# Kernel tuning notes

Measured on AMD Instinct MI355X. Metric: run time of the kernel, lower is better.

Reference implementation:

```python
import jax, jax.numpy as jnp
import numpy as np
from jax import lax

N, H, W, C = 4, 64, 64, 256
G, K = 8, 3
Cg = C // G
PAD, STRIDE, DIL = 1, 1, 1
OFFSET_SCALE = 1.0
P = K * K


def setup_inputs() -> dict:
    key = jax.random.key(0)
    ks = jax.random.split(key, 12)
    s = 1.0 / np.sqrt(C)
    return {
        "x": jax.random.normal(ks[0], (N, H, W, C), jnp.float32),
        "in_w": jax.random.normal(ks[1], (C, C), jnp.float32) * s,
        "in_b": jnp.zeros((C,), jnp.float32),
        "out_w": jax.random.normal(ks[2], (C, C), jnp.float32) * s,
        "out_b": jnp.zeros((C,), jnp.float32),
        "off_w": jax.random.normal(ks[3], (C, G * P * 2), jnp.float32) * 0.02,
        "off_b": jax.random.normal(ks[4], (G * P * 2,), jnp.float32) * 0.1,
        "mask_w": jax.random.normal(ks[5], (C, G * P), jnp.float32) * 0.02,
        "mask_b": jnp.zeros((G * P,), jnp.float32),
        "dw_k": jax.random.normal(ks[6], (C, 1, K, K), jnp.float32) * (1.0 / K),
        "bn_g": 1.0 + 0.1 * jax.random.normal(ks[7], (C,), jnp.float32),
        "bn_b": 0.1 * jax.random.normal(ks[8], (C,), jnp.float32),
        "bn_m": 0.1 * jax.random.normal(ks[9], (C,), jnp.float32),
        "bn_v": 1.0 + 0.1 * jax.random.uniform(ks[10], (C,), jnp.float32),
    }


def _bilinear_sample(img, grid):
    # img: [B, Cc, Hi, Wi]; grid: [B, L, P, 2], (x, y) in [-1, 1]
    # grid_sample(mode='bilinear', padding_mode='zeros', align_corners=False)
    B, Cc, Hi, Wi = img.shape
    x = ((grid[..., 0] + 1.0) * Wi - 1.0) * 0.5
    y = ((grid[..., 1] + 1.0) * Hi - 1.0) * 0.5
    x0 = jnp.floor(x)
    y0 = jnp.floor(y)
    fx = x - x0
    fy = y - y0
    x0i = x0.astype(jnp.int32)
    y0i = y0.astype(jnp.int32)
    flat = img.reshape(B, Cc, Hi * Wi)
    gather = jax.vmap(lambda f, i: f[:, i])  # [Cc,HW], [L,P] -> [Cc,L,P]

    def corner(xc, yc, w):
        valid = (xc >= 0) & (xc < Wi) & (yc >= 0) & (yc < Hi)
        idx = jnp.clip(yc, 0, Hi - 1) * Wi + jnp.clip(xc, 0, Wi - 1)
        return gather(flat, idx) * (w * valid)[:, None]

    out = corner(x0i, y0i, (1.0 - fx) * (1.0 - fy))
    out = out + corner(x0i + 1, y0i, fx * (1.0 - fy))
    out = out + corner(x0i, y0i + 1, (1.0 - fx) * fy)
    out = out + corner(x0i + 1, y0i + 1, fx * fy)
    return out  # [B, Cc, L, P]


def reference(x, in_w, in_b, out_w, out_b, off_w, off_b, mask_w, mask_b,
              dw_k, bn_g, bn_b, bn_m, bn_v):
    # input_proj
    xp = x @ in_w + in_b  # [N,H,W,C]

    # depthwise conv (Conv: conv -> BN(inference) -> SiLU) on NCHW
    x1 = jnp.transpose(x, (0, 3, 1, 2))
    x1 = lax.conv_general_dilated(x1, dw_k, (1, 1), [(PAD, PAD), (PAD, PAD)],
                                  feature_group_count=C)
    x1 = (bn_g[:, None, None] * (x1 - bn_m[:, None, None])
          * lax.rsqrt(bn_v + 1e-5)[:, None, None] + bn_b[:, None, None])
    x1 = jax.nn.silu(x1)
    x1 = jnp.transpose(x1, (0, 2, 3, 1))  # NHWC

    offset = x1 @ off_w + off_b  # [N,H,W,G*P*2]
    mask = jax.nn.softmax((x1 @ mask_w + mask_b).reshape(N, H, W, G, P), -1)

    # dcnv3 core: pad input, compute sampling locations, bilinear gather
    Hi, Wi = H + 2 * PAD, W + 2 * PAD
    xpad = jnp.pad(xp, ((0, 0), (PAD, PAD), (PAD, PAD), (0, 0)))

    base = (DIL * (K - 1)) // 2 + 0.5
    ref_y = (base + jnp.arange(H, dtype=jnp.float32) * STRIDE) / Hi
    ref_x = (base + jnp.arange(W, dtype=jnp.float32) * STRIDE) / Wi
    ref = jnp.stack(jnp.meshgrid(ref_x, ref_y, indexing="xy"), -1)  # [H,W,2]

    g1 = jnp.arange(K, dtype=jnp.float32) * DIL - (DIL * (K - 1)) // 2
    gx = jnp.repeat(g1 / Wi, K)  # kx outer (torch meshgrid 'ij' order)
    gy = jnp.tile(g1 / Hi, K)    # ky inner
    grid = jnp.stack([gx, gy], -1)  # [P,2]

    norm = jnp.array([Wi, Hi], jnp.float32)
    loc = (ref[None, :, :, None, None, :]
           + grid[None, None, None, None, :, :] * OFFSET_SCALE
           + offset.reshape(N, H, W, G, P, 2) * (OFFSET_SCALE / norm))
    sgrid = 2.0 * loc - 1.0  # [N,H,W,G,P,2]

    img = xpad.reshape(N, Hi * Wi, G, Cg).transpose(0, 2, 3, 1).reshape(N * G, Cg, Hi, Wi)
    sg = sgrid.reshape(N, H * W, G, P, 2).transpose(0, 2, 1, 3, 4).reshape(N * G, H * W, P, 2)
    samples = _bilinear_sample(img, sg)  # [N*G, Cg, L, P]
    m = mask.reshape(N, H * W, G, P).transpose(0, 2, 1, 3).reshape(N * G, 1, H * W, P)
    out = (samples * m).sum(-1)  # [N*G, Cg, L]
    out = out.reshape(N, C, H * W).transpose(0, 2, 1).reshape(N, H, W, C)
    return out @ out_w + out_b
```

## Files before the change

kernel.cpp:

```cpp
#include <hip/hip_runtime.h>
#include <math.h>

#define NB   4
#define HH   64
#define WW   64
#define CCH  256
#define GG   8
#define CGC  32
#define HI   66
#define NPIX 16384
#define OMWS 256

typedef unsigned short ushort_t;
typedef __attribute__((ext_vector_type(8))) short short8;
typedef __attribute__((ext_vector_type(4))) float floatx4;

__device__ inline ushort_t f2bf(float f) {
    union { float f; unsigned u; } v; v.f = f;
    unsigned r = v.u + 0x7FFF + ((v.u >> 16) & 1);
    return (ushort_t)(r >> 16);
}
__device__ inline float bf2f(ushort_t u) {
    union { unsigned u; float f; } v; v.u = ((unsigned)u) << 16; return v.f;
}

__device__ inline void gload_lds16(const ushort_t* g, ushort_t* l) {
    __builtin_amdgcn_global_load_lds(
        (const __attribute__((address_space(1))) void*)g,
        (__attribute__((address_space(3))) void*)l, 16, 0, 0);
}

template<int MODE>
__device__ __forceinline__
void gemm_body(const ushort_t* __restrict__ A, const ushort_t* __restrict__ Bt,
               const float* __restrict__ bias, void* __restrict__ outv,
               ushort_t* As, ushort_t* Bs, int row0, int col0)
{
    const int tid  = threadIdx.x;
    const int lane = tid & 63, wid = tid >> 6;
    const int q = lane >> 4, r = lane & 15;

    floatx4 acc[2][4] = {};

    auto stage = [&](int buf, int kt) {
        #pragma unroll
        for (int j = 0; j < 4; ++j) {
            int gi = j * 256 + tid;
            int arow = gi >> 3, gk = gi & 7;
            gload_lds16(A + (size_t)(row0 + arow) * 256 + kt * 64 + ((gk ^ (arow & 7)) * 8),
                        &As[buf * 128 * 64 + gi * 8]);
        }
        #pragma unroll
        for (int j = 0; j < 2; ++j) {
            int gi = j * 256 + tid;
            int brow = gi >> 3, gk = gi & 7;
            gload_lds16(Bt + (size_t)(col0 + brow) * 256 + kt * 64 + ((gk ^ (brow & 7)) * 8),
                        &Bs[buf * 64 * 64 + gi * 8]);
        }
    };

    stage(0, 0);
    __syncthreads();
    int cur = 0;
    #pragma unroll 1
    for (int kt = 0; kt < 4; ++kt) {
        if (kt < 3) stage(cur ^ 1, kt + 1);
        #pragma unroll
        for (int kk = 0; kk < 2; ++kk) {
            short8 af[2], bf[4];
            const int gsw = ((kk * 4 + q) ^ (r & 7)) * 8;
            #pragma unroll
            for (int m = 0; m < 2; ++m)
                af[m] = *(const short8*)&As[cur * 128 * 64 + (wid * 32 + m * 16 + r) * 64 + gsw];
            #pragma unroll
            for (int n = 0; n < 4; ++n)
                bf[n] = *(const short8*)&Bs[cur * 64 * 64 + (n * 16 + r) * 64 + gsw];
            #pragma unroll
            for (int m = 0; m < 2; ++m)
                #pragma unroll
                for (int n = 0; n < 4; ++n)
                    acc[m][n] = __builtin_amdgcn_mfma_f32_16x16x32_bf16(
                                    af[m], bf[n], acc[m][n], 0, 0, 0);
        }
        __syncthreads();
        cur ^= 1;
    }

    #pragma unroll
    for (int m = 0; m < 2; ++m) {
        #pragma unroll
        for (int n = 0; n < 4; ++n) {
            #pragma unroll
            for (int j = 0; j < 4; ++j) {
                int row = row0 + wid * 32 + m * 16 + q * 4 + j;
                int col = col0 + n * 16 + r;
                float v = acc[m][n][j] + bias[col];
                if (MODE == 1) {
                    int nn = row >> 12, hh = (row >> 6) & 63, www = row & 63;
                    ((ushort_t*)outv)[(size_t)((nn * HI + hh + 1) * HI + (www + 1)) * CCH + col] = f2bf(v);
                } else if (MODE == 2) {
                    ((ushort_t*)outv)[(size_t)row * 256 + col] = f2bf(v);
                } else {
                    ((float*)outv)[(size_t)row * 256 + col] = v;
                }
            }
        }
    }
}

__device__ __forceinline__ void swz512(int tbid, int& row0, int& col0) {
    int swz = (tbid & 7) * 64 + (tbid >> 3);
    row0 = (swz >> 2) * 128;
    col0 = (swz & 3) * 64;
}

__global__ __launch_bounds__(256)
void gemm_in_off(const ushort_t* __restrict__ xb, const ushort_t* __restrict__ WtIn,
                 const float* __restrict__ in_b, ushort_t* __restrict__ xpadb,
                 const ushort_t* __restrict__ x1b, const ushort_t* __restrict__ W2t,
                 const float* __restrict__ b2, ushort_t* __restrict__ offm)
{
    __shared__ ushort_t As[2 * 128 * 64];
    __shared__ ushort_t Bs[2 * 64 * 64];
    int bid = blockIdx.x;
    int row0, col0;
    if (bid < 512) {
        swz512(bid, row0, col0);
        gemm_body<1>(xb, WtIn, in_b, xpadb, As, Bs, row0, col0);
    } else {
        swz512(bid - 512, row0, col0);
        gemm_body<2>(x1b, W2t, b2, offm, As, Bs, row0, col0);
    }
}

__global__ __launch_bounds__(256)
void gemm_out(const ushort_t* __restrict__ A, const ushort_t* __restrict__ Bt,
              const float* __restrict__ bias, float* __restrict__ out)
{
    __shared__ ushort_t As[2 * 128 * 64];
    __shared__ ushort_t Bs[2 * 64 * 64];
    int row0, col0;
    swz512(blockIdx.x, row0, col0);
    gemm_body<0>(A, Bt, bias, out, As, Bs, row0, col0);
}

__global__ __launch_bounds__(256)
void prep_dw(const float* __restrict__ x,
             const float* __restrict__ in_w, const float* __restrict__ out_w,
             const float* __restrict__ off_w, const float* __restrict__ mask_w,
             const float* __restrict__ off_b, const float* __restrict__ mask_b,
             const float* __restrict__ dw_k, const float* __restrict__ bn_g,
             const float* __restrict__ bn_b, const float* __restrict__ bn_m,
             const float* __restrict__ bn_v,
             ushort_t* __restrict__ xpadb,
             ushort_t* __restrict__ WtIn, ushort_t* __restrict__ WtOut,
             ushort_t* __restrict__ W2t, float* __restrict__ b2,
             ushort_t* __restrict__ x1b, ushort_t* __restrict__ xb)
{
    __shared__ float kT[9][256];
    const int bid = blockIdx.x;
    const int tid = threadIdx.x;

    if (bid < NB * 260) {
        int n = bid / 260, rp = bid % 260;
        int h, w;
        if (rp < 66)       { h = 0;              w = rp; }
        else if (rp < 132) { h = 65;             w = rp - 66; }
        else if (rp < 196) { h = 1 + (rp - 132); w = 0; }
        else               { h = 1 + (rp - 196); w = 65; }
        xpadb[(size_t)((n * HI + h) * HI + w) * CCH + tid] = 0;
        return;
    }
    if (bid < NB * 260 + 256) {
        int n = bid - NB * 260, k = tid;
        WtIn [n * 256 + k] = f2bf(in_w [k * 256 + n]);
        WtOut[n * 256 + k] = f2bf(out_w[k * 256 + n]);
        float w2 = (n < 144) ? off_w[k * 144 + n]
                 : (n < 216) ? mask_w[k * 72 + (n - 144)] : 0.f;
        W2t[n * 256 + k] = f2bf(w2);
        if (k == 0) b2[n] = (n < 144) ? off_b[n] : (n < 216) ? mask_b[n - 144] : 0.f;
        return;
    }

    #pragma unroll
    for (int j = 0; j < 9; ++j) {
        int i = j * 256 + tid;
        kT[i % 9][i / 9] = dw_k[i];
    }
    __syncthreads();

    const int lane = tid & 63, wvid = tid >> 6;
    const int pix = (bid - (NB * 260 + 256)) * 4 + wvid;
    const int n = pix >> 12, hw = pix & 4095, h = hw >> 6, w = hw & 63;
    const int c4 = lane << 2;

    const float4 cv = *reinterpret_cast<const float4*>(x + (size_t)pix * CCH + c4);
    ushort_t xo[4] = { f2bf(cv.x), f2bf(cv.y), f2bf(cv.z), f2bf(cv.w) };
    *reinterpret_cast<ushort4*>(xb + (size_t)pix * CCH + c4) = *reinterpret_cast<ushort4*>(xo);

    const float4 kc = *reinterpret_cast<const float4*>(&kT[4][c4]);
    float ax = cv.x * kc.x, ay = cv.y * kc.y, az = cv.z * kc.z, aw = cv.w * kc.w;

    #pragma unroll
    for (int tap = 0; tap < 9; ++tap) {
        if (tap == 4) continue;
        int hh = h + tap / 3 - 1, ww = w + tap % 3 - 1;
        if ((unsigned)hh < HH && (unsigned)ww < WW) {
            const float4 v = *reinterpret_cast<const float4*>(
                x + (size_t)((n * HH + hh) * WW + ww) * CCH + c4);
            const float4 kk = *reinterpret_cast<const float4*>(&kT[tap][c4]);
            ax += v.x * kk.x; ay += v.y * kk.y; az += v.z * kk.z; aw += v.w * kk.w;
        }
    }
    const float4 g4 = *reinterpret_cast<const float4*>(bn_g + c4);
    const float4 v4 = *reinterpret_cast<const float4*>(bn_v + c4);
    const float4 m4 = *reinterpret_cast<const float4*>(bn_m + c4);
    const float4 bb4 = *reinterpret_cast<const float4*>(bn_b + c4);
    float sx = g4.x * rsqrtf(v4.x + 1e-5f), sy = g4.y * rsqrtf(v4.y + 1e-5f);
    float sz = g4.z * rsqrtf(v4.z + 1e-5f), sw = g4.w * rsqrtf(v4.w + 1e-5f);
    float yx = (ax - m4.x) * sx + bb4.x, yy = (ay - m4.y) * sy + bb4.y;
    float yz = (az - m4.z) * sz + bb4.z, yw = (aw - m4.w) * sw + bb4.w;
    yx = yx / (1.f + __expf(-yx));
    yy = yy / (1.f + __expf(-yy));
    yz = yz / (1.f + __expf(-yz));
    yw = yw / (1.f + __expf(-yw));
    ushort_t o[4] = { f2bf(yx), f2bf(yy), f2bf(yz), f2bf(yw) };
    *reinterpret_cast<ushort4*>(x1b + (size_t)pix * CCH + c4) = *reinterpret_cast<ushort4*>(o);
}

__global__ __launch_bounds__(256)
void dcn_sample(const ushort_t* __restrict__ xpadb, const ushort_t* __restrict__ om,
                ushort_t* __restrict__ coreb)
{
    const int tid = threadIdx.x;
    const int pix = blockIdx.x * 8 + (tid >> 5);
    const int l   = tid & 31;
    const int g = l >> 2, c8 = (l & 3) << 3;
    const int n = pix >> 12, hw = pix & 4095, h = hw >> 6, w = hw & 63;
    const ushort_t* __restrict__ omp = om + (size_t)pix * OMWS;

    float lg[9], mx = -1e30f;
    #pragma unroll
    for (int p = 0; p < 9; ++p) { lg[p] = bf2f(omp[144 + g * 9 + p]); mx = fmaxf(mx, lg[p]); }
    float s = 0.f;
    #pragma unroll
    for (int p = 0; p < 9; ++p) { lg[p] = __expf(lg[p] - mx); s += lg[p]; }
    const float inv = 1.f / s;

    const ushort_t* __restrict__ img = xpadb + (size_t)n * HI * HI * CCH + g * CGC + c8;
    float acc[8] = {};
    #pragma unroll
    for (int p = 0; p < 9; ++p) {
        float ox = bf2f(omp[g * 18 + p * 2 + 0]);
        float oy = bf2f(omp[g * 18 + p * 2 + 1]);
        float xi = (float)(w + (p / 3)) + ox;
        float yi = (float)(h + (p % 3)) + oy;
        float x0f = floorf(xi), y0f = floorf(yi);
        int x0 = (int)x0f, y0 = (int)y0f;
        float fx = xi - x0f, fy = yi - y0f;
        float wgt = lg[p] * inv;
        float cw[4] = { (1.f - fx) * (1.f - fy) * wgt, fx * (1.f - fy) * wgt,
                        (1.f - fx) * fy * wgt,         fx * fy * wgt };
        #pragma unroll
        for (int cr = 0; cr < 4; ++cr) {
            int xc = x0 + (cr & 1), yc = y0 + (cr >> 1);
            if ((unsigned)xc < HI && (unsigned)yc < HI) {
                short8 raw = *reinterpret_cast<const short8*>(img + (size_t)(yc * HI + xc) * CCH);
                float wc = cw[cr];
                #pragma unroll
                for (int j = 0; j < 8; ++j) acc[j] += wc * bf2f((ushort_t)raw[j]);
            }
        }
    }
    ushort_t o[8];
    #pragma unroll
    for (int j = 0; j < 8; ++j) o[j] = f2bf(acc[j]);
    *reinterpret_cast<short8*>(coreb + (size_t)pix * CCH + g * CGC + c8) =
        *reinterpret_cast<short8*>(o);
}

extern "C" void kernel_launch(void* const* d_in, const int* in_sizes, int n_in,
                              void* d_out, int out_size, void* d_ws, size_t ws_size,
                              hipStream_t stream) {
    const float* x      = (const float*)d_in[0];
    const float* in_w   = (const float*)d_in[1];
    const float* in_b   = (const float*)d_in[2];
    const float* out_w  = (const float*)d_in[3];
    const float* out_b  = (const float*)d_in[4];
    const float* off_w  = (const float*)d_in[5];
    const float* off_b  = (const float*)d_in[6];
    const float* mask_w = (const float*)d_in[7];
    const float* mask_b = (const float*)d_in[8];
    const float* dw_k   = (const float*)d_in[9];
    const float* bn_g   = (const float*)d_in[10];
    const float* bn_b   = (const float*)d_in[11];
    const float* bn_m   = (const float*)d_in[12];
    const float* bn_v   = (const float*)d_in[13];

    ushort_t* xpadb = (ushort_t*)d_ws;
    ushort_t* xb    = xpadb + 4460544;
    ushort_t* x1b   = xb + 4194304;
    ushort_t* coreb = x1b + 4194304;
    ushort_t* offm  = coreb + 4194304;
    ushort_t* WtIn  = offm + 4194304;
    ushort_t* WtOut = WtIn + 65536;
    ushort_t* W2t   = WtOut + 65536;
    float*    b2    = (float*)(W2t + 65536);

    prep_dw<<<NB * 260 + 256 + NPIX / 4, 256, 0, stream>>>(x,
        in_w, out_w, off_w, mask_w, off_b, mask_b,
        dw_k, bn_g, bn_b, bn_m, bn_v,
        xpadb, WtIn, WtOut, W2t, b2, x1b, xb);

    gemm_in_off<<<1024, 256, 0, stream>>>(xb, WtIn, in_b, xpadb, x1b, W2t, b2, offm);

    dcn_sample<<<NPIX / 8, 256, 0, stream>>>(xpadb, offm, coreb);

    gemm_out<<<512, 256, 0, stream>>>(coreb, WtOut, out_b, (float*)d_out);
}
```

Before: 61.00 us.

## Stage per-group 16x16 input window in LDS for deformable sampling

Restructures the sampling kernel so that each block handles one 8x8 spatial tile for a single group and batch item. The block first loads a 16x16 halo window of the padded input (32 channels) into shared memory, and bilinear corner fetches inside the window read from LDS. Corners outside the window fall back to global loads. This is meant to replace repeated scattered global and L2 reads with LDS reuse across neighbouring pixels. The cost is an extra sync, 16KB of LDS per block, and strided per-group reads of the offset/mask rows.

```diff
diff --git a/kernel.cpp b/kernel.cpp
--- a/kernel.cpp
+++ b/kernel.cpp
@@ -229,14 +229,35 @@
 }
 
 __global__ __launch_bounds__(256)
-void dcn_sample(const ushort_t* __restrict__ xpadb, const ushort_t* __restrict__ om,
-                ushort_t* __restrict__ coreb)
-{
+void dcn_tile(const ushort_t* __restrict__ xpadb, const ushort_t* __restrict__ om,
+              ushort_t* __restrict__ coreb)
+{
+    __shared__ ushort_t win[4 * 256 * 8];
     const int tid = threadIdx.x;
-    const int pix = blockIdx.x * 8 + (tid >> 5);
-    const int l   = tid & 31;
-    const int g = l >> 2, c8 = (l & 3) << 3;
-    const int n = pix >> 12, hw = pix & 4095, h = hw >> 6, w = hw & 63;
+    const int bid = blockIdx.x;
+    const int tx = bid & 7, ty = (bid >> 3) & 7, g = (bid >> 6) & 7, n = bid >> 9;
+    const int wx0 = tx * 8 - 3, wy0 = ty * 8 - 3;
+
+    {
+        const int dy = tid >> 4, dx = tid & 15;
+        const int yy = wy0 + dy, xx = wx0 + dx;
+        short8 v[4] = {{0,0,0,0,0,0,0,0},{0,0,0,0,0,0,0,0},
+                       {0,0,0,0,0,0,0,0},{0,0,0,0,0,0,0,0}};
+        if ((unsigned)yy < HI && (unsigned)xx < HI) {
+            const ushort_t* src = xpadb + (size_t)((n * HI + yy) * HI + xx) * CCH + g * CGC;
+            #pragma unroll
+            for (int gr = 0; gr < 4; ++gr)
+                v[gr] = *reinterpret_cast<const short8*>(src + gr * 8);
+        }
+        #pragma unroll
+        for (int gr = 0; gr < 4; ++gr)
+            *reinterpret_cast<short8*>(&win[(gr * 256 + tid) * 8]) = v[gr];
+    }
+    __syncthreads();
+
+    const int px = tid >> 2, gr = tid & 3;
+    const int h = ty * 8 + (px >> 3), w = tx * 8 + (px & 7);
+    const int pix = (n << 12) | (h << 6) | w;
     const ushort_t* __restrict__ omp = om + (size_t)pix * OMWS;
 
     float lg[9], mx = -1e30f;
@@ -247,7 +268,6 @@
     for (int p = 0; p < 9; ++p) { lg[p] = __expf(lg[p] - mx); s += lg[p]; }
     const float inv = 1.f / s;
 
-    const ushort_t* __restrict__ img = xpadb + (size_t)n * HI * HI * CCH + g * CGC + c8;
     float acc[8] = {};
     #pragma unroll
     for (int p = 0; p < 9; ++p) {
@@ -264,9 +284,16 @@
         #pragma unroll
         for (int cr = 0; cr < 4; ++cr) {
             int xc = x0 + (cr & 1), yc = y0 + (cr >> 1);
-            if ((unsigned)xc < HI && (unsigned)yc < HI) {
-                short8 raw = *reinterpret_cast<const short8*>(img + (size_t)(yc * HI + xc) * CCH);
-                float wc = cw[cr];
+            int sx = xc - wx0, sy = yc - wy0;
+            float wc = cw[cr];
+            if ((unsigned)sx < 16 && (unsigned)sy < 16) {
+                short8 raw = *reinterpret_cast<const short8*>(
+                    &win[(gr * 256 + sy * 16 + sx) * 8]);
+                #pragma unroll
+                for (int j = 0; j < 8; ++j) acc[j] += wc * bf2f((ushort_t)raw[j]);
+            } else if ((unsigned)xc < HI && (unsigned)yc < HI) {
+                short8 raw = *reinterpret_cast<const short8*>(
+                    xpadb + (size_t)((n * HI + yc) * HI + xc) * CCH + g * CGC + gr * 8);
                 #pragma unroll
                 for (int j = 0; j < 8; ++j) acc[j] += wc * bf2f((ushort_t)raw[j]);
             }
@@ -275,7 +302,7 @@
     ushort_t o[8];
     #pragma unroll
     for (int j = 0; j < 8; ++j) o[j] = f2bf(acc[j]);
-    *reinterpret_cast<short8*>(coreb + (size_t)pix * CCH + g * CGC + c8) =
+    *reinterpret_cast<short8*>(coreb + (size_t)pix * CCH + g * CGC + gr * 8) =
         *reinterpret_cast<short8*>(o);
 }
 
@@ -314,7 +341,7 @@
 
     gemm_in_off<<<1024, 256, 0, stream>>>(xb, WtIn, in_b, xpadb, x1b, W2t, b2, offm);
 
-    dcn_sample<<<NPIX / 8, 256, 0, stream>>>(xpadb, offm, coreb);
+    dcn_tile<<<NB * GG * 64, 256, 0, stream>>>(xpadb, offm, coreb);
 
     gemm_out<<<512, 256, 0, stream>>>(coreb, WtOut, out_b, (float*)d_out);
 }
```

Measured after the change: 58.37 us. 4.3% less time.
